# Kernel optimization log

Measured on AMD Instinct MI355X. Metric: run time of the kernel, lower is better.

Reference implementation:

```python
import jax, jax.numpy as jnp
import numpy as np

PATCH = 64      # patch_size
K = 16          # num_patches
UNF_K = 16      # unfold kernel
UNF_S = 8       # unfold stride


def setup_inputs() -> dict:
    key = jax.random.key(0)
    k0, k1, k2 = jax.random.split(key, 3)
    B, C, H, W = 32, 3, 384, 384
    x = jax.random.normal(k0, (B, C, H, W), dtype=jnp.float32)
    # encoder params: Conv2d(3,32,3,s2,p1) -> ReLU -> Conv2d(32,64,3,s2,p1) -> GAP
    w1 = jax.random.normal(k1, (32, 3, 3, 3), dtype=jnp.float32) * 0.1
    b1 = jnp.zeros((32,), dtype=jnp.float32)
    w2 = jax.random.normal(k2, (64, 32, 3, 3), dtype=jnp.float32) * 0.05
    b2 = jnp.zeros((64,), dtype=jnp.float32)
    return {"x": x, "w1": w1, "b1": b1, "w2": w2, "b2": b2}


def _patch_variances(x):
    # torch.var(unfold(x,16,8), dim=1), unbiased, over C*16*16 = 768 elems.
    # Computed via window sums instead of materializing the unfold tensor.
    win = (1, 1, UNF_K, UNF_K)
    st = (1, 1, UNF_S, UNF_S)
    s = jax.lax.reduce_window(x, 0.0, jax.lax.add, win, st, 'VALID')
    s2 = jax.lax.reduce_window(x * x, 0.0, jax.lax.add, win, st, 'VALID')
    s = s.sum(axis=1)    # [B, gh, gw]
    s2 = s2.sum(axis=1)  # [B, gh, gw]
    n = x.shape[1] * UNF_K * UNF_K  # 768
    var = (s2 - s * s / n) / (n - 1)
    return var.reshape(var.shape[0], -1)  # [B, gh*gw], row-major like F.unfold


def _encode(patches, w1, b1, w2, b2):
    # patches: [N, 3, 64, 64] -> [N, 64]
    dn = ('NCHW', 'OIHW', 'NCHW')
    y = jax.lax.conv_general_dilated(patches, w1, (2, 2), [(1, 1), (1, 1)],
                                     dimension_numbers=dn) + b1[None, :, None, None]
    y = jax.nn.relu(y)
    y = jax.lax.conv_general_dilated(y, w2, (2, 2), [(1, 1), (1, 1)],
                                     dimension_numbers=dn) + b2[None, :, None, None]
    return y.mean(axis=(2, 3))  # AdaptiveAvgPool2d(1)


def reference(x, w1, b1, w2, b2):
    B, C, H, W = x.shape
    var = _patch_variances(x)                 # [B, L]
    _, idx = jax.lax.top_k(var, K)            # [B, K]
    # faithful (buggy) decode from the source: divisor is W//8, step 8
    h = (idx // (W // UNF_S)) * UNF_S         # [B, K]
    w = (idx % (W // UNF_S)) * UNF_S          # [B, K]

    def slice_one(img, hh, ww):
        # dynamic_slice clamps starts so the 64x64 crop stays in-bounds
        return jax.lax.dynamic_slice(img, (0, hh, ww), (C, PATCH, PATCH))

    gather = jax.vmap(lambda img, hs, ws: jax.vmap(
        lambda hh, ww: slice_one(img, hh, ww))(hs, ws))
    patches = gather(x, h, w)                 # [B, K, 3, 64, 64]
    feats = _encode(patches.reshape(B * K, C, PATCH, PATCH), w1, b1, w2, b2)
    return feats.reshape(B, K, -1).mean(axis=1)  # [B, 64]
```

## Files before the change

kernel.cpp:

```cpp
#include <hip/hip_runtime.h>
#include <math.h>

#define NB 32
#define GH 47
#define GW 47
#define NWIN (GH*GW)
#define KSEL 16
#define RPITCH 17

__global__ __launch_bounds__(256) void k_var(const float* __restrict__ x,
                                             float* __restrict__ var)
{
    __shared__ double hs [3][24][GW];
    __shared__ double hs2[3][24][GW];
    int gyp = blockIdx.x;
    int b   = blockIdx.y;
    int tid = threadIdx.x;
    int R0  = gyp * 16;

    for (int tau = tid; tau < 3*24*GW; tau += 256) {
        int gx = tau % GW;
        int t2 = tau / GW;
        int rr = t2 % 24;
        int c  = t2 / 24;
        int row = R0 + rr;
        double s = 0.0, s2 = 0.0;
        if (row < 384) {
            const float* px = x + (((size_t)(b*3 + c)*384 + row)*384 + gx*8);
            #pragma unroll
            for (int q = 0; q < 4; ++q) {
                float4 v = *reinterpret_cast<const float4*>(px + q*4);
                double a0 = v.x, a1 = v.y, a2 = v.z, a3 = v.w;
                s  += a0 + a1 + a2 + a3;
                s2 = fma(a0,a0, fma(a1,a1, fma(a2,a2, fma(a3,a3, s2))));
            }
        }
        hs [c][rr][gx] = s;
        hs2[c][rr][gx] = s2;
    }
    __syncthreads();

    int w = tid;
    if (w < 2*GW) {
        int g = w / GW, gx = w % GW;
        int gy = gyp*2 + g;
        if (gy < GH) {
            double S = 0.0, S2 = 0.0;
            #pragma unroll
            for (int c = 0; c < 3; ++c)
                #pragma unroll
                for (int r = 0; r < 16; ++r) {
                    S  += hs [c][g*8 + r][gx];
                    S2 += hs2[c][g*8 + r][gx];
                }
            var[(size_t)b*NWIN + gy*GW + gx] =
                (float)((S2 - S*S/768.0) / 767.0);
        }
    }
}

__global__ void k_topk(const float* __restrict__ var, int* __restrict__ coords)
{
    int b = blockIdx.x, l = threadIdx.x;
    unsigned long long key[35];
    #pragma unroll
    for (int j = 0; j < 35; ++j) {
        int idx = j*64 + l;
        unsigned long long kk = 0ULL;
        if (idx < NWIN) {
            unsigned u = __float_as_uint(var[(size_t)b*NWIN + idx]);
            unsigned mono = u ^ ((unsigned)((int)u >> 31) | 0x80000000u);
            kk = ((unsigned long long)mono << 12) | (unsigned)(4095 - idx);
        }
        key[j] = kk;
    }
    for (int it = 0; it < KSEL; ++it) {
        unsigned long long bk = 0ULL;
        #pragma unroll
        for (int j = 0; j < 35; ++j) bk = key[j] > bk ? key[j] : bk;
        #pragma unroll
        for (int m = 1; m < 64; m <<= 1) {
            unsigned long long o = __shfl_xor(bk, m, 64);
            bk = o > bk ? o : bk;
        }
        #pragma unroll
        for (int j = 0; j < 35; ++j) if (key[j] == bk) key[j] = 0ULL;
        if (l == 0) {
            int idx = 4095 - (int)(bk & 0xFFFULL);
            int h = (idx / 48) * 8; if (h > 320) h = 320;
            int w = (idx % 48) * 8; if (w > 320) w = 320;
            coords[(b*KSEL + it)*2 + 0] = h;
            coords[(b*KSEL + it)*2 + 1] = w;
        }
    }
}

__global__ __launch_bounds__(256, 2) void k_encode(const float* __restrict__ x,
    const float* __restrict__ w1, const float* __restrict__ b1,
    const int* __restrict__ coords, float* __restrict__ sbuf)
{
    __shared__ float4 sin4[3*66*RPITCH];
    __shared__ float  s_S[32*9];

    int p    = blockIdx.x;
    int bimg = p >> 4;
    int tid  = threadIdx.x;
    int h0 = coords[p*2 + 0];
    int w0 = coords[p*2 + 1];

    float4 z4 = make_float4(0.f, 0.f, 0.f, 0.f);
    for (int i = tid; i < 3*66*RPITCH; i += 256) sin4[i] = z4;
    __syncthreads();

    float* sinf = (float*)sin4;
    #pragma unroll
    for (int it = 0; it < 12; ++it) {
        int fi  = tid + it*256;
        int c   = fi >> 10;
        int rem = fi & 1023;
        int y   = rem >> 4;
        int x4  = rem & 15;
        float4 v = *reinterpret_cast<const float4*>(
            x + (((size_t)(bimg*3 + c)*384 + (h0 + y))*384 + w0 + x4*4));
        int r  = y + 1;
        int sw = (r >> 1) & 7;
        float vals[4] = {v.x, v.y, v.z, v.w};
        #pragma unroll
        for (int e = 0; e < 4; ++e) {
            int pcol = x4*4 + 1 + e;
            int k  = pcol >> 2, bb = pcol & 3;
            int ks = (k < 16) ? ((k & 8) | ((k & 7) ^ sw)) : 16;
            sinf[((c*66 + r)*RPITCH + ks)*4 + bb] = vals[e];
        }
    }
    __syncthreads();

    int lane = tid & 63;
    int iy   = lane >> 1;
    int xh   = lane & 1;
    int icg  = __builtin_amdgcn_readfirstlane(tid >> 6);

    float acc[8][16];
    #pragma unroll
    for (int i = 0; i < 8; ++i)
        #pragma unroll
        for (int t = 0; t < 16; ++t) acc[i][t] = 0.f;

    const float* w1g = w1 + icg*8*27;

    for (int ch = 0; ch < 3; ++ch) {
        for (int ky = 0; ky < 3; ++ky) {
            int r    = 2*iy + ky;
            int sw   = (r >> 1) & 7;
            int base = (ch*66 + r)*RPITCH;
            float s[33];
            #pragma unroll
            for (int j = 0; j < 8; ++j) {
                float4 v = sin4[base + (8*xh | (j ^ sw))];
                s[4*j+0] = v.x; s[4*j+1] = v.y; s[4*j+2] = v.z; s[4*j+3] = v.w;
            }
            {
                int k  = 8*xh + 8;
                int ks = (k < 16) ? ((k & 8) | ((k & 7) ^ sw)) : 16;
                s[32] = sinf[(base + ks)*4];
            }
            const float* wp = w1g + ch*9 + ky*3;
            #pragma unroll
            for (int i = 0; i < 8; ++i) {
                float wA = wp[i*27 + 0];
                float wB = wp[i*27 + 1];
                float wC = wp[i*27 + 2];
                #pragma unroll
                for (int t = 0; t < 16; ++t)
                    acc[i][t] = fmaf(s[2*t], wA,
                                 fmaf(s[2*t+1], wB,
                                  fmaf(s[2*t+2], wC, acc[i][t])));
            }
        }
    }

    float R[8][3];
    #pragma unroll
    for (int i = 0; i < 8; ++i) {
        float bias = b1[icg*8 + i];
        float c1 = 0.f, c2 = 0.f, vlast = 0.f;
        #pragma unroll
        for (int t = 0; t < 16; ++t) {
            float v = fmaxf(acc[i][t] + bias, 0.f);
            if (t & 1) c2 += v; else c1 += v;
            if (t == 15) vlast = v;
        }
        R[i][0] = c2 - (xh ? vlast : 0.f);
        R[i][1] = c1;
        R[i][2] = c2;
    }

    #pragma unroll
    for (int i = 0; i < 8; ++i)
        #pragma unroll
        for (int k = 0; k < 3; ++k)
            R[i][k] += __shfl_xor(R[i][k], 1, 64);

    float c31[8][3];
    #pragma unroll
    for (int i = 0; i < 8; ++i)
        #pragma unroll
        for (int k = 0; k < 3; ++k)
            c31[i][k] = __shfl(R[i][k], 62, 64);

    #pragma unroll
    for (int m = 4; m < 64; m <<= 1)
        #pragma unroll
        for (int i = 0; i < 8; ++i)
            #pragma unroll
            for (int k = 0; k < 3; ++k)
                R[i][k] += __shfl_xor(R[i][k], m, 64);

    if (lane == 0) {
        #pragma unroll
        for (int i = 0; i < 8; ++i)
            #pragma unroll
            for (int k = 0; k < 3; ++k)
                s_S[(icg*8 + i)*9 + 3 + k] = R[i][k];
    } else if (lane == 2) {
        #pragma unroll
        for (int i = 0; i < 8; ++i)
            #pragma unroll
            for (int k = 0; k < 3; ++k) {
                s_S[(icg*8 + i)*9 + 0 + k] = R[i][k] - c31[i][k];
                s_S[(icg*8 + i)*9 + 6 + k] = R[i][k];
            }
    }
    __syncthreads();

    for (int i = tid; i < 288; i += 256)
        sbuf[(size_t)p*288 + i] = s_S[i];
}

__global__ __launch_bounds__(256) void k_reduce(const float* __restrict__ sbuf,
    const float* __restrict__ w2, const float* __restrict__ b2,
    float* __restrict__ out)
{
    __shared__ float Ssum[288];
    __shared__ float s_part[256];
    int b = blockIdx.x, tid = threadIdx.x;

    for (int i = tid; i < 288; i += 256) {
        float s = 0.f;
        #pragma unroll
        for (int k = 0; k < KSEL; ++k)
            s += sbuf[(size_t)(b*KSEL + k)*288 + i];
        Ssum[i] = s;
    }
    __syncthreads();

    int oc = tid & 63, q = tid >> 6;
    const float4* w4 = reinterpret_cast<const float4*>(w2 + oc*288 + q*72);
    const float4* S4 = reinterpret_cast<const float4*>(Ssum + q*72);
    float a = 0.f;
    #pragma unroll
    for (int t = 0; t < 18; ++t) {
        float4 wv = w4[t];
        float4 sv = S4[t];
        a = fmaf(wv.x, sv.x, fmaf(wv.y, sv.y,
             fmaf(wv.z, sv.z, fmaf(wv.w, sv.w, a))));
    }
    s_part[tid] = a;
    __syncthreads();
    if (tid < 64) {
        float t = s_part[tid] + s_part[64 + tid] + s_part[128 + tid] + s_part[192 + tid];
        out[b*64 + tid] = b2[tid] + t * (1.0f/4096.0f);
    }
}

extern "C" void kernel_launch(void* const* d_in, const int* in_sizes, int n_in,
                              void* d_out, int out_size, void* d_ws, size_t ws_size,
                              hipStream_t stream)
{
    const float* x  = (const float*)d_in[0];
    const float* w1 = (const float*)d_in[1];
    const float* b1 = (const float*)d_in[2];
    const float* w2 = (const float*)d_in[3];
    const float* b2 = (const float*)d_in[4];
    float* out = (float*)d_out;

    char* ws = (char*)d_ws;
    int*   coords = (int*)ws;
    float* var    = (float*)(ws + 4096);
    float* sbuf   = (float*)(ws + 4096);

    k_var   <<<dim3(24, NB), 256, 0, stream>>>(x, var);
    k_topk  <<<NB,            64, 0, stream>>>(var, coords);
    k_encode<<<NB*KSEL,      256, 0, stream>>>(x, w1, b1, coords, sbuf);
    k_reduce<<<NB,           256, 0, stream>>>(sbuf, w2, b2, out);
}
```

Measured before the change: 73.81 us.

## Fuse top-k selection into encode kernel and halve per-row sums in variance kernel

```diff
diff --git a/kernel.cpp b/kernel.cpp
--- a/kernel.cpp
+++ b/kernel.cpp
@@ -7,110 +7,120 @@
 #define NWIN (GH*GW)
 #define KSEL 16
 #define RPITCH 17
+#define SEG 48
 
 __global__ __launch_bounds__(256) void k_var(const float* __restrict__ x,
                                              float* __restrict__ var)
 {
-    __shared__ double hs [3][24][GW];
-    __shared__ double hs2[3][24][GW];
+    __shared__ double hs [3][24][SEG];
+    __shared__ double hs2[3][24][SEG];
     int gyp = blockIdx.x;
     int b   = blockIdx.y;
     int tid = threadIdx.x;
     int R0  = gyp * 16;
 
-    for (int tau = tid; tau < 3*24*GW; tau += 256) {
-        int gx = tau % GW;
-        int t2 = tau / GW;
+    for (int tau = tid; tau < 3*24*SEG; tau += 256) {
+        int sg = tau % SEG;
+        int t2 = tau / SEG;
         int rr = t2 % 24;
         int c  = t2 / 24;
         int row = R0 + rr;
         double s = 0.0, s2 = 0.0;
         if (row < 384) {
-            const float* px = x + (((size_t)(b*3 + c)*384 + row)*384 + gx*8);
-            #pragma unroll
-            for (int q = 0; q < 4; ++q) {
+            const float* px = x + (((size_t)(b*3 + c)*384 + row)*384 + sg*8);
+            #pragma unroll
+            for (int q = 0; q < 2; ++q) {
                 float4 v = *reinterpret_cast<const float4*>(px + q*4);
                 double a0 = v.x, a1 = v.y, a2 = v.z, a3 = v.w;
                 s  += a0 + a1 + a2 + a3;
                 s2 = fma(a0,a0, fma(a1,a1, fma(a2,a2, fma(a3,a3, s2))));
             }
         }
-        hs [c][rr][gx] = s;
-        hs2[c][rr][gx] = s2;
-    }
-    __syncthreads();
-
-    int w = tid;
-    if (w < 2*GW) {
-        int g = w / GW, gx = w % GW;
+        hs [c][rr][sg] = s;
+        hs2[c][rr][sg] = s2;
+    }
+    __syncthreads();
+
+    if (tid < 188) {
+        int which = tid & 1;
+        int rest  = tid >> 1;
+        int gx = rest % 47, g = rest / 47;
         int gy = gyp*2 + g;
         if (gy < GH) {
-            double S = 0.0, S2 = 0.0;
+            const double* base = which ? &hs2[0][0][0] : &hs[0][0][0];
+            double S = 0.0;
             #pragma unroll
             for (int c = 0; c < 3; ++c)
                 #pragma unroll
                 for (int r = 0; r < 16; ++r) {
-                    S  += hs [c][g*8 + r][gx];
-                    S2 += hs2[c][g*8 + r][gx];
+                    const double* rp = base + ((c*24) + (g*8 + r))*SEG + gx;
+                    S += rp[0] + rp[1];
                 }
-            var[(size_t)b*NWIN + gy*GW + gx] =
-                (float)((S2 - S*S/768.0) / 767.0);
+            double P = __shfl_xor(S, 1, 64);
+            if (which == 0) {
+                var[(size_t)b*NWIN + gy*GW + gx] =
+                    (float)((P - S*S/768.0) / 767.0);
+            }
         }
     }
 }
 
-__global__ void k_topk(const float* __restrict__ var, int* __restrict__ coords)
+__global__ __launch_bounds__(256, 2) void k_encode(const float* __restrict__ x,
+    const float* __restrict__ w1, const float* __restrict__ b1,
+    const float* __restrict__ var, float* __restrict__ sbuf)
 {
-    int b = blockIdx.x, l = threadIdx.x;
-    unsigned long long key[35];
-    #pragma unroll
-    for (int j = 0; j < 35; ++j) {
-        int idx = j*64 + l;
-        unsigned long long kk = 0ULL;
-        if (idx < NWIN) {
-            unsigned u = __float_as_uint(var[(size_t)b*NWIN + idx]);
-            unsigned mono = u ^ ((unsigned)((int)u >> 31) | 0x80000000u);
-            kk = ((unsigned long long)mono << 12) | (unsigned)(4095 - idx);
-        }
-        key[j] = kk;
-    }
-    for (int it = 0; it < KSEL; ++it) {
+    __shared__ float4 sin4[3*66*RPITCH];
+    __shared__ float  s_S[32*9];
+    __shared__ int    s_hw[2];
+
+    int p    = blockIdx.x;
+    int bimg = p >> 4;
+    int krank = p & 15;
+    int tid  = threadIdx.x;
+
+    if (tid < 64) {
+        int l = tid;
+        const float* vb = var + (size_t)bimg*NWIN;
+        unsigned long long key[35];
+        #pragma unroll
+        for (int j = 0; j < 35; ++j) {
+            int idx = j*64 + l;
+            unsigned long long kk = 0ULL;
+            if (idx < NWIN) {
+                unsigned u = __float_as_uint(vb[idx]);
+                unsigned mono = u ^ ((unsigned)((int)u >> 31) | 0x80000000u);
+                kk = ((unsigned long long)mono << 12) | (unsigned)(4095 - idx);
+            }
+            key[j] = kk;
+        }
         unsigned long long bk = 0ULL;
-        #pragma unroll
-        for (int j = 0; j < 35; ++j) bk = key[j] > bk ? key[j] : bk;
-        #pragma unroll
-        for (int m = 1; m < 64; m <<= 1) {
-            unsigned long long o = __shfl_xor(bk, m, 64);
-            bk = o > bk ? o : bk;
-        }
-        #pragma unroll
-        for (int j = 0; j < 35; ++j) if (key[j] == bk) key[j] = 0ULL;
+        for (int it = 0; ; ++it) {
+            bk = 0ULL;
+            #pragma unroll
+            for (int j = 0; j < 35; ++j) bk = key[j] > bk ? key[j] : bk;
+            #pragma unroll
+            for (int m = 1; m < 64; m <<= 1) {
+                unsigned long long o = __shfl_xor(bk, m, 64);
+                bk = o > bk ? o : bk;
+            }
+            if (it == krank) break;
+            #pragma unroll
+            for (int j = 0; j < 35; ++j) if (key[j] == bk) key[j] = 0ULL;
+        }
         if (l == 0) {
             int idx = 4095 - (int)(bk & 0xFFFULL);
             int h = (idx / 48) * 8; if (h > 320) h = 320;
             int w = (idx % 48) * 8; if (w > 320) w = 320;
-            coords[(b*KSEL + it)*2 + 0] = h;
-            coords[(b*KSEL + it)*2 + 1] = w;
-        }
-    }
-}
-
-__global__ __launch_bounds__(256, 2) void k_encode(const float* __restrict__ x,
-    const float* __restrict__ w1, const float* __restrict__ b1,
-    const int* __restrict__ coords, float* __restrict__ sbuf)
-{
-    __shared__ float4 sin4[3*66*RPITCH];
-    __shared__ float  s_S[32*9];
-
-    int p    = blockIdx.x;
-    int bimg = p >> 4;
-    int tid  = threadIdx.x;
-    int h0 = coords[p*2 + 0];
-    int w0 = coords[p*2 + 1];
-
-    float4 z4 = make_float4(0.f, 0.f, 0.f, 0.f);
-    for (int i = tid; i < 3*66*RPITCH; i += 256) sin4[i] = z4;
-    __syncthreads();
+            s_hw[0] = h; s_hw[1] = w;
+        }
+    } else {
+        float4 z4 = make_float4(0.f, 0.f, 0.f, 0.f);
+        for (int i = tid - 64; i < 3*66*RPITCH; i += 192) sin4[i] = z4;
+    }
+    __syncthreads();
+
+    int h0 = s_hw[0];
+    int w0 = s_hw[1];
 
     float* sinf = (float*)sin4;
     #pragma unroll
@@ -285,12 +295,10 @@
     float* out = (float*)d_out;
 
     char* ws = (char*)d_ws;
-    int*   coords = (int*)ws;
-    float* var    = (float*)(ws + 4096);
-    float* sbuf   = (float*)(ws + 4096);
+    float* var  = (float*)ws;
+    float* sbuf = (float*)(ws + 283904);
 
     k_var   <<<dim3(24, NB), 256, 0, stream>>>(x, var);
-    k_topk  <<<NB,            64, 0, stream>>>(var, coords);
-    k_encode<<<NB*KSEL,      256, 0, stream>>>(x, w1, b1, coords, sbuf);
+    k_encode<<<NB*KSEL,      256, 0, stream>>>(x, w1, b1, var, sbuf);
     k_reduce<<<NB,           256, 0, stream>>>(sbuf, w2, b2, out);
 }
```

Result: faster. 66.27 us (-10.2%).
